# Kernel tuning notes

Measured on AMD Instinct MI355X. Metric: run time of the kernel, lower is better.

The kernel has to match this reference:

```python
import jax, jax.numpy as jnp
import numpy as np

N = 50000
E = 800000
D_IN = 1000
D_H2 = 128  # h_dim * multiple
D_H = 16


def gat_conv(x, src, dst, W, attn_l, attn_r, bias, n):
    """DGL-style GATConv (no dropout, no activation). Returns [n, H, F]."""
    H, F = attn_l.shape
    feat = (x @ W).reshape(n, H, F)                      # [N,H,F]
    el = jnp.sum(feat * attn_l[None], axis=-1)           # [N,H]
    er = jnp.sum(feat * attn_r[None], axis=-1)           # [N,H]
    e = jax.nn.leaky_relu(el[src] + er[dst], 0.2)        # [E,H]
    emax = jax.ops.segment_max(e, dst, num_segments=n)   # [N,H] per-dst softmax max
    ee = jnp.exp(e - emax[dst])                          # [E,H]
    denom = jax.ops.segment_sum(ee, dst, num_segments=n) # [N,H]
    alpha = ee / denom[dst]                              # [E,H]
    msg = feat[src] * alpha[..., None]                   # [E,H,F]
    out = jax.ops.segment_sum(msg, dst, num_segments=n)  # [N,H,F]
    return out + bias.reshape(1, H, F)


def setup_inputs() -> dict:
    key = jax.random.key(0)
    ks = jax.random.split(key, 24)
    rn = lambda k, shp, s=0.05: (jax.random.normal(k, shp, dtype=jnp.float32) * s)
    inp = {
        "x": rn(ks[0], (N, D_IN), 1.0),
        "src": jax.random.randint(ks[1], (E,), 0, N, dtype=jnp.int32),
        "dst": jax.random.randint(ks[2], (E,), 0, N, dtype=jnp.int32),
        "W1": rn(ks[3], (D_IN, D_H2)),
        "al1": rn(ks[4], (1, D_H2)),
        "ar1": rn(ks[5], (1, D_H2)),
        "b1": jnp.zeros((D_H2,), jnp.float32),
        "W2": rn(ks[6], (D_H2, 2 * D_H2)),
        "al2": rn(ks[7], (2, D_H2)),
        "ar2": rn(ks[8], (2, D_H2)),
        "b2": jnp.zeros((2 * D_H2,), jnp.float32),
        "Wm": rn(ks[9], (D_H2, 2 * D_H)),
        "alm": rn(ks[10], (2, D_H)),
        "arm": rn(ks[11], (2, D_H)),
        "bm": jnp.zeros((2 * D_H,), jnp.float32),
        "Wv": rn(ks[12], (D_H2, 2 * D_H)),
        "alv": rn(ks[13], (2, D_H)),
        "arv": rn(ks[14], (2, D_H)),
        "bv": jnp.zeros((2 * D_H,), jnp.float32),
        "eps": rn(ks[15], (N, D_H), 1.0),
    }
    return inp


def reference(x, src, dst, W1, al1, ar1, b1, W2, al2, ar2, b2,
              Wm, alm, arm, bm, Wv, alv, arv, bv, eps):
    n = x.shape[0]
    o = gat_conv(x, src, dst, W1, al1, ar1, b1, n).mean(-2)           # [N,128]
    o = gat_conv(o, src, dst, W2, al2, ar2, b2, n).mean(-2) + o       # residual
    mean = gat_conv(o, src, dst, Wm, alm, arm, bm, n).mean(-2)        # [N,16]
    var = jnp.exp(gat_conv(o, src, dst, Wv, alv, arv, bv, n).mean(-2))
    z = mean + jnp.sqrt(var) * eps                                    # reparameterize
    return z, mean, var
```

## Files before the change

kernel.cpp:

```cpp
#include <hip/hip_runtime.h>
#include <hip/hip_bf16.h>
#include <math.h>

typedef unsigned short u16;
typedef unsigned int u32;
typedef __attribute__((ext_vector_type(8))) __bf16 bf16x8;
typedef __attribute__((ext_vector_type(4))) float f32x4;
typedef __attribute__((ext_vector_type(4))) u32 u32x4;
typedef __attribute__((ext_vector_type(2))) u32 u32x2;

#define NNODES 50000
#define NEDGES 800000

__device__ __forceinline__ float bf2f(u16 u) {
    union { u32 i; float f; } v; v.i = ((u32)u) << 16; return v.f;
}
__device__ __forceinline__ u16 f2bf(float x) {
    union { float f; u32 i; } v; v.f = x;
    u32 r = v.i + 0x7fffu + ((v.i >> 16) & 1u);
    return (u16)(r >> 16);
}
__device__ __forceinline__ float lrelu(float x) { return x >= 0.f ? x : 0.2f * x; }

__global__ __launch_bounds__(256) void k_zero2(int* a, int* b, int count) {
    int i = blockIdx.x * 256 + threadIdx.x;
    if (i < count) { a[i] = 0; b[i] = 0; }
}

__global__ __launch_bounds__(256) void k_count(const int* __restrict__ dst, int* __restrict__ counts, int e) {
    int i = blockIdx.x * 256 + threadIdx.x;
    if (i < e) atomicAdd(&counts[dst[i]], 1);
}

__global__ __launch_bounds__(256) void k_scan1(const int* __restrict__ counts, int* __restrict__ row_ptr,
                                               int* __restrict__ bsums, int n) {
    __shared__ int tmp[256];
    int t = threadIdx.x, i = blockIdx.x * 256 + t;
    int v = (i < n) ? counts[i] : 0;
    tmp[t] = v; __syncthreads();
    for (int off = 1; off < 256; off <<= 1) {
        int x = 0; if (t >= off) x = tmp[t - off];
        __syncthreads(); tmp[t] += x; __syncthreads();
    }
    if (i < n) row_ptr[i] = tmp[t] - v;
    if (t == 255) bsums[blockIdx.x] = tmp[255];
}

__global__ __launch_bounds__(256) void k_scan2(int* bsums, int nb) {
    __shared__ int tmp[256];
    int t = threadIdx.x;
    int v = (t < nb) ? bsums[t] : 0;
    tmp[t] = v; __syncthreads();
    for (int off = 1; off < 256; off <<= 1) {
        int x = 0; if (t >= off) x = tmp[t - off];
        __syncthreads(); tmp[t] += x; __syncthreads();
    }
    if (t < nb) bsums[t] = tmp[t] - v;
}

__global__ __launch_bounds__(256) void k_scan3(int* __restrict__ row_ptr, const int* __restrict__ bsums,
                                               int n, int total) {
    int i = blockIdx.x * 256 + threadIdx.x;
    if (i < n) row_ptr[i] += bsums[blockIdx.x];
    if (i == 0) row_ptr[n] = total;
}

__global__ __launch_bounds__(256) void k_fill(const int* __restrict__ src, const int* __restrict__ dst,
                                              const int* __restrict__ row_ptr, int* __restrict__ cursor,
                                              int* __restrict__ esrc, int e) {
    int i = blockIdx.x * 256 + threadIdx.x;
    if (i < e) {
        int d = dst[i];
        int p = row_ptr[d] + atomicAdd(&cursor[d], 1);
        esrc[p] = src[i];
    }
}

__global__ __launch_bounds__(256) void k_prep(const float* __restrict__ W1, const float* __restrict__ W2,
                                              const float* __restrict__ Wm, const float* __restrict__ Wv,
                                              const float* __restrict__ al2, const float* __restrict__ ar2,
                                              const float* __restrict__ b2,
                                              u16* __restrict__ W1t, u16* __restrict__ Wct,
                                              u16* __restrict__ Bmvt,
                                              float* __restrict__ ul, float* __restrict__ ur,
                                              float* __restrict__ bmean) {
    int b = blockIdx.x, t = threadIdx.x;
    if (b < 500) {
        int i = b * 256 + t;
        int k = i >> 7, n = i & 127;
        W1t[(size_t)n * 1000 + k] = f2bf(W1[i]);
    } else if (b < 628) {
        int i = (b - 500) * 256 + t;
        int f = i >> 8, c = i & 255, h = c >> 7, k = c & 127;
        Wct[i] = f2bf(0.5f * W2[(size_t)k * 256 + h * 128 + f]);
    } else if (b == 628) {
        int h = t >> 7, k = t & 127;
        const float* wrow = W2 + (size_t)k * 256 + h * 128;
        const float* alh = al2 + h * 128;
        const float* arh = ar2 + h * 128;
        float sl = 0.f, sr = 0.f;
        for (int f = 0; f < 128; f += 4) {
            f32x4 w = *(const f32x4*)(wrow + f);
            f32x4 a = *(const f32x4*)(alh + f);
            f32x4 r = *(const f32x4*)(arh + f);
#pragma unroll
            for (int q = 0; q < 4; q++) { sl += w[q] * a[q]; sr += w[q] * r[q]; }
        }
        ul[t] = sl; ur[t] = sr;
        if (t < 128) bmean[t] = 0.5f * (b2[t] + b2[128 + t]);
    } else {
        for (int i = t; i < 64 * 128; i += 256) {
            int c = i >> 7, k = i & 127;
            Bmvt[i] = f2bf(c < 32 ? Wm[(size_t)k * 32 + c] : Wv[(size_t)k * 32 + (c - 32)]);
        }
    }
}

__device__ __forceinline__ void load_af(const float* __restrict__ arow, int k0, int K, bf16x8& a) {
    if (k0 + 8 <= K) {
        f32x4 a0 = *(const f32x4*)(arow + k0);
        f32x4 a1 = *(const f32x4*)(arow + k0 + 4);
#pragma unroll
        for (int j = 0; j < 4; j++) { a[j] = (__bf16)a0[j]; a[4 + j] = (__bf16)a1[j]; }
    } else {
#pragma unroll
        for (int j = 0; j < 8; j++) a[j] = (__bf16)0.f;
    }
}
__device__ __forceinline__ void load_af(const u16* __restrict__ arow, int k0, int K, bf16x8& a) {
    if (k0 + 8 <= K) a = *(const bf16x8*)(arow + k0);
    else {
#pragma unroll
        for (int j = 0; j < 8; j++) a[j] = (__bf16)0.f;
    }
}

template <typename AT, int MODE>
__global__ __launch_bounds__(256) void k_gemm_tiled(const AT* __restrict__ A, const u16* __restrict__ Bt,
                                                    u16* __restrict__ C, int M, int Nn, int K,
                                                    const float* __restrict__ bias,
                                                    const u16* __restrict__ resid,
                                                    const float* __restrict__ al,
                                                    const float* __restrict__ ar,
                                                    float* __restrict__ el, float* __restrict__ er) {
    __shared__ __align__(16) u16 lb[2][128 * 40];
    const int tid = threadIdx.x;
    const int wave = tid >> 6, lane = tid & 63;
    const int m = lane & 15, quad = lane >> 4;
    const int row0 = blockIdx.x * 64 + wave * 16;
    const int col0 = blockIdx.y * 128;

    f32x4 acc[8];
#pragma unroll
    for (int t = 0; t < 8; t++)
#pragma unroll
        for (int r = 0; r < 4; r++) acc[t][r] = 0.f;

    int arr = row0 + m; if (arr > M - 1) arr = M - 1;
    const AT* arow = A + (size_t)arr * K;
    const int scol = tid & 127;
    const int sseg = (tid >> 7) * 16;
    const u16* bcol = Bt + (size_t)(col0 + scol) * K;

    const int nsteps = (K + 31) >> 5;

#pragma unroll
    for (int p = 0; p < 2; ++p) {
        int kl = sseg + p * 8;
        u32x4 v = 0;
        if (kl < K) v = *(const u32x4*)(bcol + kl);
        *(u32x4*)&lb[0][scol * 40 + kl] = v;
    }
    bf16x8 acur, anext;
    load_af(arow, quad * 8, K, acur);
    __syncthreads();

    for (int s = 0; s < nsteps; ++s) {
        const int buf = s & 1;
        if (s + 1 < nsteps) {
            const int k0n = (s + 1) * 32;
            load_af(arow, k0n + quad * 8, K, anext);
#pragma unroll
            for (int p = 0; p < 2; ++p) {
                int kl = sseg + p * 8;
                u32x4 v = 0;
                if (k0n + kl < K) v = *(const u32x4*)(bcol + k0n + kl);
                *(u32x4*)&lb[buf ^ 1][scol * 40 + kl] = v;
            }
        }
#pragma unroll
        for (int t = 0; t < 8; ++t) {
            bf16x8 b = *(const bf16x8*)&lb[buf][(t * 16 + m) * 40 + quad * 8];
            acc[t] = __builtin_amdgcn_mfma_f32_16x16x32_bf16(acur, b, acc[t], 0, 0, 0);
        }
        acur = anext;
        __syncthreads();
    }

#pragma unroll
    for (int r = 0; r < 4; r++) {
        int row = row0 + quad * 4 + r;
        if (MODE == 0) {
            float pe = 0.f, pr = 0.f;
#pragma unroll
            for (int t = 0; t < 8; t++) {
                float a = acc[t][r];
                int c = col0 + t * 16 + m;
                pe += a * al[c]; pr += a * ar[c];
            }
#pragma unroll
            for (int off = 8; off; off >>= 1) { pe += __shfl_xor(pe, off); pr += __shfl_xor(pr, off); }
            if (m == 0 && row < M) { el[row] = pe; er[row] = pr; }
        }
#pragma unroll
        for (int t = 0; t < 8; t++) {
            int col = col0 + t * 16 + m;
            if (row < M) {
                float v = acc[t][r];
                if (MODE == 1) v += bias[col] + bf2f(resid[(size_t)row * Nn + col]);
                C[(size_t)row * Nn + col] = f2bf(v);
            }
        }
    }
}

__global__ __launch_bounds__(64) void k_gemmmv(const u16* __restrict__ A, const u16* __restrict__ Bt,
                                               u16* __restrict__ featmv,
                                               const float* __restrict__ alm, const float* __restrict__ arm,
                                               const float* __restrict__ alv, const float* __restrict__ arv,
                                               float* __restrict__ elm, float* __restrict__ erm,
                                               float* __restrict__ elv, float* __restrict__ erv, int M) {
    int row0 = blockIdx.x * 16;
    int lane = threadIdx.x;
    int m = lane & 15, quad = lane >> 4;
    f32x4 acc[4];
#pragma unroll
    for (int t = 0; t < 4; t++)
#pragma unroll
        for (int r = 0; r < 4; r++) acc[t][r] = 0.f;

    const u16* arow = A + (size_t)(row0 + m) * 128 + quad * 8;
#pragma unroll
    for (int s = 0; s < 4; ++s) {
        bf16x8 a = *(const bf16x8*)(arow + s * 32);
#pragma unroll
        for (int t = 0; t < 4; t++) {
            bf16x8 b = *(const bf16x8*)(Bt + (size_t)(t * 16 + m) * 128 + s * 32 + quad * 8);
            acc[t] = __builtin_amdgcn_mfma_f32_16x16x32_bf16(a, b, acc[t], 0, 0, 0);
        }
    }
#pragma unroll
    for (int r = 0; r < 4; r++) {
        int row = row0 + quad * 4 + r;
#pragma unroll
        for (int t = 0; t < 4; t++) {
            float a = acc[t][r];
            const float* alp = (t < 2) ? alm : alv;
            const float* arp = (t < 2) ? arm : arv;
            float pe = a * alp[(t & 1) * 16 + m];
            float pr = a * arp[(t & 1) * 16 + m];
#pragma unroll
            for (int off = 8; off; off >>= 1) { pe += __shfl_xor(pe, off); pr += __shfl_xor(pr, off); }
            if (m == 0 && row < M) {
                float* elp = (t < 2) ? elm : elv;
                float* erp = (t < 2) ? erm : erv;
                elp[row * 2 + (t & 1)] = pe; erp[row * 2 + (t & 1)] = pr;
            }
            if (row < M) featmv[(size_t)row * 64 + t * 16 + m] = f2bf(a);
        }
    }
}

__global__ __launch_bounds__(256) void k_agg1(const int* __restrict__ row_ptr, const int* __restrict__ esrc,
                                              const u16* __restrict__ feat, const float* __restrict__ el,
                                              const float* __restrict__ er, const float* __restrict__ bias,
                                              const float* __restrict__ ul, const float* __restrict__ ur,
                                              u16* __restrict__ o_bf, float* __restrict__ el2,
                                              float* __restrict__ er2, int n) {
    int wave = threadIdx.x >> 6, lane = threadIdx.x & 63;
    int l = lane & 31;
    int node = blockIdx.x * 8 + wave * 2 + (lane >> 5);
    if (node >= n) node = n - 1;
    int beg = row_ptr[node], deg = row_ptr[node + 1] - beg;
    float erd = er[node];
    int degmax = max(deg, __shfl_xor(deg, 32));
    const int srcb = lane & 32;
    float acc0 = 0.f, acc1 = 0.f, acc2 = 0.f, acc3 = 0.f, den = 0.f;
    for (int off0 = 0; off0 < degmax; off0 += 32) {
        float w = 0.f; int s = 0;
        if (off0 + l < deg) { s = esrc[beg + off0 + l]; w = expf(lrelu(el[s] + erd)); }
        den += w;
        int cnt = min(32, degmax - off0);
        int j = 0;
        for (; j + 4 <= cnt; j += 4) {
            int s0 = __shfl(s, srcb + j),     s1 = __shfl(s, srcb + j + 1);
            int s2 = __shfl(s, srcb + j + 2), s3 = __shfl(s, srcb + j + 3);
            float w0 = __shfl(w, srcb + j),     w1 = __shfl(w, srcb + j + 1);
            float w2 = __shfl(w, srcb + j + 2), w3 = __shfl(w, srcb + j + 3);
            u32x2 p0 = ((const u32x2*)(feat + (size_t)s0 * 128))[l];
            u32x2 p1 = ((const u32x2*)(feat + (size_t)s1 * 128))[l];
            u32x2 p2 = ((const u32x2*)(feat + (size_t)s2 * 128))[l];
            u32x2 p3 = ((const u32x2*)(feat + (size_t)s3 * 128))[l];
            acc0 += w0 * bf2f((u16)(p0.x & 0xffff)) + w1 * bf2f((u16)(p1.x & 0xffff))
                  + w2 * bf2f((u16)(p2.x & 0xffff)) + w3 * bf2f((u16)(p3.x & 0xffff));
            acc1 += w0 * bf2f((u16)(p0.x >> 16)) + w1 * bf2f((u16)(p1.x >> 16))
                  + w2 * bf2f((u16)(p2.x >> 16)) + w3 * bf2f((u16)(p3.x >> 16));
            acc2 += w0 * bf2f((u16)(p0.y & 0xffff)) + w1 * bf2f((u16)(p1.y & 0xffff))
                  + w2 * bf2f((u16)(p2.y & 0xffff)) + w3 * bf2f((u16)(p3.y & 0xffff));
            acc3 += w0 * bf2f((u16)(p0.y >> 16)) + w1 * bf2f((u16)(p1.y >> 16))
                  + w2 * bf2f((u16)(p2.y >> 16)) + w3 * bf2f((u16)(p3.y >> 16));
        }
        for (; j < cnt; ++j) {
            int sj = __shfl(s, srcb + j);
            float wj = __shfl(w, srcb + j);
            u32x2 pv = ((const u32x2*)(feat + (size_t)sj * 128))[l];
            acc0 += wj * bf2f((u16)(pv.x & 0xffff));
            acc1 += wj * bf2f((u16)(pv.x >> 16));
            acc2 += wj * bf2f((u16)(pv.y & 0xffff));
            acc3 += wj * bf2f((u16)(pv.y >> 16));
        }
    }
#pragma unroll
    for (int off = 16; off; off >>= 1) den += __shfl_xor(den, off);
    float inv = (den > 0.f) ? 1.f / den : 0.f;
    const int c0 = 4 * l;
    float o0 = acc0 * inv + bias[c0];
    float o1 = acc1 * inv + bias[c0 + 1];
    float o2 = acc2 * inv + bias[c0 + 2];
    float o3 = acc3 * inv + bias[c0 + 3];
#pragma unroll
    for (int h = 0; h < 2; ++h) {
        const float* ulh = ul + h * 128 + c0;
        const float* urh = ur + h * 128 + c0;
        float pe = o0 * ulh[0] + o1 * ulh[1] + o2 * ulh[2] + o3 * ulh[3];
        float pr = o0 * urh[0] + o1 * urh[1] + o2 * urh[2] + o3 * urh[3];
#pragma unroll
        for (int off = 16; off; off >>= 1) { pe += __shfl_xor(pe, off); pr += __shfl_xor(pr, off); }
        if (l == 0) { el2[node * 2 + h] = pe; er2[node * 2 + h] = pr; }
    }
    u32x2 pv;
    pv.x = (u32)f2bf(o0) | ((u32)f2bf(o1) << 16);
    pv.y = (u32)f2bf(o2) | ((u32)f2bf(o3) << 16);
    ((u32x2*)(o_bf + (size_t)node * 128))[l] = pv;
}

__global__ __launch_bounds__(256) void k_agg2o(const int* __restrict__ row_ptr, const int* __restrict__ esrc,
                                               const u16* __restrict__ o_in, const float* __restrict__ el,
                                               const float* __restrict__ er, u16* __restrict__ agg, int n) {
    int wave = threadIdx.x >> 6, lane = threadIdx.x & 63;
    int l = lane & 31;
    int node = blockIdx.x * 8 + wave * 2 + (lane >> 5);
    if (node >= n) node = n - 1;
    int beg = row_ptr[node], deg = row_ptr[node + 1] - beg;
    float er0 = er[node * 2], er1 = er[node * 2 + 1];
    int degmax = max(deg, __shfl_xor(deg, 32));
    const int srcb = lane & 32;
    float a00 = 0.f, a01 = 0.f, a02 = 0.f, a03 = 0.f;
    float a10 = 0.f, a11 = 0.f, a12 = 0.f, a13 = 0.f;
    float d0 = 0.f, d1 = 0.f;
    for (int off0 = 0; off0 < degmax; off0 += 32) {
        float w0 = 0.f, w1 = 0.f; int s = 0;
        if (off0 + l < deg) {
            s = esrc[beg + off0 + l];
            float2 e2 = *(const float2*)(el + 2 * s);
            w0 = expf(lrelu(e2.x + er0));
            w1 = expf(lrelu(e2.y + er1));
        }
        d0 += w0; d1 += w1;
        int cnt = min(32, degmax - off0);
        int j = 0;
        for (; j + 2 <= cnt; j += 2) {
            int sa = __shfl(s, srcb + j), sb = __shfl(s, srcb + j + 1);
            float w0a = __shfl(w0, srcb + j), w0b = __shfl(w0, srcb + j + 1);
            float w1a = __shfl(w1, srcb + j), w1b = __shfl(w1, srcb + j + 1);
            u32x2 pa = ((const u32x2*)(o_in + (size_t)sa * 128))[l];
            u32x2 pb = ((const u32x2*)(o_in + (size_t)sb * 128))[l];
            float fa0 = bf2f((u16)(pa.x & 0xffff)), fa1 = bf2f((u16)(pa.x >> 16));
            float fa2 = bf2f((u16)(pa.y & 0xffff)), fa3 = bf2f((u16)(pa.y >> 16));
            float fb0 = bf2f((u16)(pb.x & 0xffff)), fb1 = bf2f((u16)(pb.x >> 16));
            float fb2 = bf2f((u16)(pb.y & 0xffff)), fb3 = bf2f((u16)(pb.y >> 16));
            a00 += w0a * fa0 + w0b * fb0;  a01 += w0a * fa1 + w0b * fb1;
            a02 += w0a * fa2 + w0b * fb2;  a03 += w0a * fa3 + w0b * fb3;
            a10 += w1a * fa0 + w1b * fb0;  a11 += w1a * fa1 + w1b * fb1;
            a12 += w1a * fa2 + w1b * fb2;  a13 += w1a * fa3 + w1b * fb3;
        }
        for (; j < cnt; ++j) {
            int sj = __shfl(s, srcb + j);
            float w0j = __shfl(w0, srcb + j), w1j = __shfl(w1, srcb + j);
            u32x2 pv = ((const u32x2*)(o_in + (size_t)sj * 128))[l];
            float f0 = bf2f((u16)(pv.x & 0xffff)), f1 = bf2f((u16)(pv.x >> 16));
            float f2 = bf2f((u16)(pv.y & 0xffff)), f3 = bf2f((u16)(pv.y >> 16));
            a00 += w0j * f0; a01 += w0j * f1; a02 += w0j * f2; a03 += w0j * f3;
            a10 += w1j * f0; a11 += w1j * f1; a12 += w1j * f2; a13 += w1j * f3;
        }
    }
#pragma unroll
    for (int off = 16; off; off >>= 1) { d0 += __shfl_xor(d0, off); d1 += __shfl_xor(d1, off); }
    float i0 = (d0 > 0.f) ? 1.f / d0 : 0.f, i1 = (d1 > 0.f) ? 1.f / d1 : 0.f;
    u32x2 p0, p1;
    p0.x = (u32)f2bf(a00 * i0) | ((u32)f2bf(a01 * i0) << 16);
    p0.y = (u32)f2bf(a02 * i0) | ((u32)f2bf(a03 * i0) << 16);
    p1.x = (u32)f2bf(a10 * i1) | ((u32)f2bf(a11 * i1) << 16);
    p1.y = (u32)f2bf(a12 * i1) | ((u32)f2bf(a13 * i1) << 16);
    u32x2* aw = (u32x2*)(agg + (size_t)node * 256);
    aw[l] = p0;
    aw[32 + l] = p1;
}

__global__ __launch_bounds__(256) void k_aggmv(const int* __restrict__ row_ptr, const int* __restrict__ esrc,
                                               const u16* __restrict__ featmv,
                                               const float* __restrict__ elm, const float* __restrict__ erm,
                                               const float* __restrict__ elv, const float* __restrict__ erv,
                                               const float* __restrict__ bm, const float* __restrict__ bv,
                                               const float* __restrict__ eps, float* __restrict__ out, int n) {
    int wave = threadIdx.x >> 6, lane = threadIdx.x & 63;
    int l = lane & 31;
    int node = blockIdx.x * 8 + wave * 2 + (lane >> 5);
    if (node >= n) node = n - 1;
    int tbl = l >> 4, h = (l >> 3) & 1;
    int beg = row_ptr[node], deg = row_ptr[node + 1] - beg;
    float erm0 = erm[2 * node], erm1 = erm[2 * node + 1];
    float erv0 = erv[2 * node], erv1 = erv[2 * node + 1];
    int degmax = max(deg, __shfl_xor(deg, 32));
    const int srcb = lane & 32;
    float acc0 = 0.f, acc1 = 0.f;
    float dm0 = 0.f, dm1 = 0.f, dv0 = 0.f, dv1 = 0.f;
    for (int off0 = 0; off0 < degmax; off0 += 32) {
        float wm0 = 0.f, wm1 = 0.f, wv0 = 0.f, wv1 = 0.f; int s = 0;
        if (off0 + l < deg) {
            s = esrc[beg + off0 + l];
            float2 em = *(const float2*)(elm + 2 * s);
            float2 ev = *(const float2*)(elv + 2 * s);
            wm0 = expf(lrelu(em.x + erm0));
            wm1 = expf(lrelu(em.y + erm1));
            wv0 = expf(lrelu(ev.x + erv0));
            wv1 = expf(lrelu(ev.y + erv1));
        }
        dm0 += wm0; dm1 += wm1; dv0 += wv0; dv1 += wv1;
        int cnt = min(32, degmax - off0);
        int j = 0;
        for (; j + 2 <= cnt; j += 2) {
            int sa = __shfl(s, srcb + j), sb = __shfl(s, srcb + j + 1);
            float am0 = __shfl(wm0, srcb + j), bm0_ = __shfl(wm0, srcb + j + 1);
            float am1 = __shfl(wm1, srcb + j), bm1_ = __shfl(wm1, srcb + j + 1);
            float av0 = __shfl(wv0, srcb + j), bv0_ = __shfl(wv0, srcb + j + 1);
            float av1 = __shfl(wv1, srcb + j), bv1_ = __shfl(wv1, srcb + j + 1);
            float wa = tbl ? (h ? av1 : av0) : (h ? am1 : am0);
            float wb = tbl ? (h ? bv1_ : bv0_) : (h ? bm1_ : bm0_);
            u32 pa = ((const u32*)(featmv + (size_t)sa * 64))[l];
            u32 pb = ((const u32*)(featmv + (size_t)sb * 64))[l];
            acc0 += wa * bf2f((u16)(pa & 0xffff)) + wb * bf2f((u16)(pb & 0xffff));
            acc1 += wa * bf2f((u16)(pa >> 16)) + wb * bf2f((u16)(pb >> 16));
        }
        for (; j < cnt; ++j) {
            int sj = __shfl(s, srcb + j);
            float b0 = __shfl(wm0, srcb + j);
            float b1 = __shfl(wm1, srcb + j);
            float b2 = __shfl(wv0, srcb + j);
            float b3 = __shfl(wv1, srcb + j);
            float wj = tbl ? (h ? b3 : b2) : (h ? b1 : b0);
            u32 pv = ((const u32*)(featmv + (size_t)sj * 64))[l];
            acc0 += wj * bf2f((u16)(pv & 0xffff));
            acc1 += wj * bf2f((u16)(pv >> 16));
        }
    }
#pragma unroll
    for (int off = 16; off; off >>= 1) {
        dm0 += __shfl_xor(dm0, off); dm1 += __shfl_xor(dm1, off);
        dv0 += __shfl_xor(dv0, off); dv1 += __shfl_xor(dv1, off);
    }
    float den = tbl ? (h ? dv1 : dv0) : (h ? dm1 : dm0);
    float inv = (den > 0.f) ? 1.f / den : 0.f;
    const int fidx0 = (2 * l) & 31;
    float bias0 = tbl ? bv[fidx0] : bm[fidx0];
    float bias1 = tbl ? bv[fidx0 + 1] : bm[fidx0 + 1];
    float outc0 = acc0 * inv + bias0;
    float outc1 = acc1 * inv + bias1;
    float hm0 = 0.5f * (outc0 + __shfl_xor(outc0, 8));
    float hm1 = 0.5f * (outc1 + __shfl_xor(outc1, 8));
    int srcv = srcb + 16 + (l & 7);
    float vp0 = __shfl(hm0, srcv);
    float vp1 = __shfl(hm1, srcv);
    if (l < 8) {
        int f0 = 2 * l;
        float var0 = expf(vp0), var1 = expf(vp1);
        float2 e2 = *(const float2*)(eps + (size_t)node * 16 + f0);
        float z0 = hm0 + sqrtf(var0) * e2.x;
        float z1 = hm1 + sqrtf(var1) * e2.y;
        size_t base = (size_t)node * 16 + f0;
        *(float2*)(out + base) = make_float2(z0, z1);
        *(float2*)(out + (size_t)NNODES * 16 + base) = make_float2(hm0, hm1);
        *(float2*)(out + (size_t)2 * NNODES * 16 + base) = make_float2(var0, var1);
    }
}

extern "C" void kernel_launch(void* const* d_in, const int* in_sizes, int n_in,
                              void* d_out, int out_size, void* d_ws, size_t ws_size,
                              hipStream_t stream) {
    const int N = NNODES, E = NEDGES;
    const float* x   = (const float*)d_in[0];
    const int* src   = (const int*)d_in[1];
    const int* dst   = (const int*)d_in[2];
    const float* W1  = (const float*)d_in[3];
    const float* al1 = (const float*)d_in[4];
    const float* ar1 = (const float*)d_in[5];
    const float* b1  = (const float*)d_in[6];
    const float* W2  = (const float*)d_in[7];
    const float* al2 = (const float*)d_in[8];
    const float* ar2 = (const float*)d_in[9];
    const float* b2  = (const float*)d_in[10];
    const float* Wm  = (const float*)d_in[11];
    const float* alm = (const float*)d_in[12];
    const float* arm = (const float*)d_in[13];
    const float* bm  = (const float*)d_in[14];
    const float* Wv  = (const float*)d_in[15];
    const float* alv = (const float*)d_in[16];
    const float* arv = (const float*)d_in[17];
    const float* bv  = (const float*)d_in[18];
    const float* eps = (const float*)d_in[19];
    float* out = (float*)d_out;

    char* ws = (char*)d_ws;
    size_t off = 0;
    auto take = [&](size_t bytes) { size_t r = off; off += (bytes + 255) & ~(size_t)255; return r; };
    int* counts   = (int*)(ws + take((size_t)N * 4));
    int* cursor   = (int*)(ws + take((size_t)N * 4));
    int* row_ptr  = (int*)(ws + take((size_t)(N + 1) * 4));
    int* bsums    = (int*)(ws + take(256 * 4));
    int* esrc     = (int*)(ws + take((size_t)E * 4));
    u16* W1t      = (u16*)(ws + take((size_t)128 * 1000 * 2));
    u16* Wct      = (u16*)(ws + take((size_t)128 * 256 * 2));
    u16* Bmvt     = (u16*)(ws + take((size_t)64 * 128 * 2));
    float* ul2    = (float*)(ws + take(256 * 4));
    float* ur2    = (float*)(ws + take(256 * 4));
    float* bmean  = (float*)(ws + take(128 * 4));
    float* el1    = (float*)(ws + take((size_t)N * 4));
    float* er1    = (float*)(ws + take((size_t)N * 4));
    float* el2    = (float*)(ws + take((size_t)N * 2 * 4));
    float* er2    = (float*)(ws + take((size_t)N * 2 * 4));
    float* elm    = (float*)(ws + take((size_t)N * 2 * 4));
    float* erm    = (float*)(ws + take((size_t)N * 2 * 4));
    float* elv    = (float*)(ws + take((size_t)N * 2 * 4));
    float* erv    = (float*)(ws + take((size_t)N * 2 * 4));
    u16* o_bf     = (u16*)(ws + take((size_t)N * 128 * 2));
    u16* o2_bf    = (u16*)(ws + take((size_t)N * 128 * 2));
    u16* R        = (u16*)(ws + take((size_t)N * 256 * 2));
    u16* feat1    = R;
    u16* agg      = R;
    u16* featmv   = R;
    (void)ws_size; (void)n_in; (void)in_sizes; (void)out_size;

    const int nb = (N + 255) / 256;
    const int eb = (E + 255) / 256;
    const int wb8 = (N + 7) / 8;
    const int gb = (N + 63) / 64;

    k_prep<<<dim3(630), 256, 0, stream>>>(W1, W2, Wm, Wv, al2, ar2, b2, W1t, Wct, Bmvt, ul2, ur2, bmean);

    k_zero2<<<dim3(nb), 256, 0, stream>>>(counts, cursor, N);
    k_count<<<dim3(eb), 256, 0, stream>>>(dst, counts, E);
    k_scan1<<<dim3(nb), 256, 0, stream>>>(counts, row_ptr, bsums, N);
    k_scan2<<<dim3(1), 256, 0, stream>>>(bsums, nb);
    k_scan3<<<dim3(nb), 256, 0, stream>>>(row_ptr, bsums, N, E);
    k_fill<<<dim3(eb), 256, 0, stream>>>(src, dst, row_ptr, cursor, esrc, E);

    k_gemm_tiled<float, 0><<<dim3(gb, 1), 256, 0, stream>>>(x, W1t, feat1, N, 128, 1000,
                                                            nullptr, nullptr, al1, ar1, el1, er1);
    k_agg1<<<dim3(wb8), 256, 0, stream>>>(row_ptr, esrc, feat1, el1, er1, b1, ul2, ur2,
                                          o_bf, el2, er2, N);

    k_agg2o<<<dim3(wb8), 256, 0, stream>>>(row_ptr, esrc, o_bf, el2, er2, agg, N);
    k_gemm_tiled<u16, 1><<<dim3(gb, 1), 256, 0, stream>>>(agg, Wct, o2_bf, N, 128, 256,
                                                          bmean, o_bf, nullptr, nullptr, nullptr, nullptr);

    k_gemmmv<<<dim3(N / 16), 64, 0, stream>>>(o2_bf, Bmvt, featmv, alm, arm, alv, arv,
                                              elm, erm, elv, erv, N);
    k_aggmv<<<dim3(wb8), 256, 0, stream>>>(row_ptr, esrc, featmv, elm, erm, elv, erv,
                                           bm, bv, eps, out, N);
}
```

Measured before the change: 577.3 us.

## Use direct global-to-LDS loads in GEMM, unroll gather, stage weights in LDS

New measurement: 577.5 us. Within noise of the previous version (+0.0%).

```diff
diff --git a/kernel.cpp b/kernel.cpp
--- a/kernel.cpp
+++ b/kernel.cpp
@@ -21,6 +21,11 @@
     return (u16)(r >> 16);
 }
 __device__ __forceinline__ float lrelu(float x) { return x >= 0.f ? x : 0.2f * x; }
+
+__device__ __forceinline__ void gload_lds16(const u16* g, u16* l) {
+    __builtin_amdgcn_global_load_lds((const __attribute__((address_space(1))) u32*)g,
+                                     (__attribute__((address_space(3))) u32*)l, 16, 0, 0);
+}
 
 __global__ __launch_bounds__(256) void k_zero2(int* a, int* b, int count) {
     int i = blockIdx.x * 256 + threadIdx.x;
@@ -143,7 +148,7 @@
                                                     const float* __restrict__ al,
                                                     const float* __restrict__ ar,
                                                     float* __restrict__ el, float* __restrict__ er) {
-    __shared__ __align__(16) u16 lb[2][128 * 40];
+    __shared__ __align__(16) u16 lb[2][4096];
     const int tid = threadIdx.x;
     const int wave = tid >> 6, lane = tid & 63;
     const int m = lane & 15, quad = lane >> 4;
@@ -158,19 +163,17 @@
 
     int arr = row0 + m; if (arr > M - 1) arr = M - 1;
     const AT* arow = A + (size_t)arr * K;
-    const int scol = tid & 127;
-    const int sseg = (tid >> 7) * 16;
-    const u16* bcol = Bt + (size_t)(col0 + scol) * K;
+    const int colA = (wave & 1) * 64 + lane;
+    const int qb = (wave >> 1) * 2;
+    const u16* bcol = Bt + (size_t)(col0 + colA) * K;
+    u16* lds0 = &lb[0][(qb * 128 + colA) * 8];
+    u16* lds1 = &lb[1][(qb * 128 + colA) * 8];
 
     const int nsteps = (K + 31) >> 5;
 
 #pragma unroll
-    for (int p = 0; p < 2; ++p) {
-        int kl = sseg + p * 8;
-        u32x4 v = 0;
-        if (kl < K) v = *(const u32x4*)(bcol + kl);
-        *(u32x4*)&lb[0][scol * 40 + kl] = v;
-    }
+    for (int p = 0; p < 2; ++p)
+        gload_lds16(bcol + (qb + p) * 8, lds0 + p * 1024);
     bf16x8 acur, anext;
     load_af(arow, quad * 8, K, acur);
     __syncthreads();
@@ -180,17 +183,16 @@
         if (s + 1 < nsteps) {
             const int k0n = (s + 1) * 32;
             load_af(arow, k0n + quad * 8, K, anext);
+            u16* ldsn = buf ? lds0 : lds1;
 #pragma unroll
             for (int p = 0; p < 2; ++p) {
-                int kl = sseg + p * 8;
-                u32x4 v = 0;
-                if (k0n + kl < K) v = *(const u32x4*)(bcol + k0n + kl);
-                *(u32x4*)&lb[buf ^ 1][scol * 40 + kl] = v;
+                int kq = k0n + (qb + p) * 8;
+                if (kq < K) gload_lds16(bcol + kq, ldsn + p * 1024);
             }
         }
 #pragma unroll
         for (int t = 0; t < 8; ++t) {
-            bf16x8 b = *(const bf16x8*)&lb[buf][(t * 16 + m) * 40 + quad * 8];
+            bf16x8 b = *(const bf16x8*)&lb[buf][(quad * 128 + t * 16 + m) * 8];
             acc[t] = __builtin_amdgcn_mfma_f32_16x16x32_bf16(acur, b, acc[t], 0, 0, 0);
         }
         acur = anext;
@@ -369,20 +371,33 @@
         d0 += w0; d1 += w1;
         int cnt = min(32, degmax - off0);
         int j = 0;
-        for (; j + 2 <= cnt; j += 2) {
-            int sa = __shfl(s, srcb + j), sb = __shfl(s, srcb + j + 1);
-            float w0a = __shfl(w0, srcb + j), w0b = __shfl(w0, srcb + j + 1);
-            float w1a = __shfl(w1, srcb + j), w1b = __shfl(w1, srcb + j + 1);
+        for (; j + 4 <= cnt; j += 4) {
+            int sa = __shfl(s, srcb + j),     sb = __shfl(s, srcb + j + 1);
+            int sc = __shfl(s, srcb + j + 2), sd = __shfl(s, srcb + j + 3);
+            float w0a = __shfl(w0, srcb + j),     w0b = __shfl(w0, srcb + j + 1);
+            float w0c = __shfl(w0, srcb + j + 2), w0d = __shfl(w0, srcb + j + 3);
+            float w1a = __shfl(w1, srcb + j),     w1b = __shfl(w1, srcb + j + 1);
+            float w1c = __shfl(w1, srcb + j + 2), w1d = __shfl(w1, srcb + j + 3);
             u32x2 pa = ((const u32x2*)(o_in + (size_t)sa * 128))[l];
             u32x2 pb = ((const u32x2*)(o_in + (size_t)sb * 128))[l];
+            u32x2 pc = ((const u32x2*)(o_in + (size_t)sc * 128))[l];
+            u32x2 pd = ((const u32x2*)(o_in + (size_t)sd * 128))[l];
             float fa0 = bf2f((u16)(pa.x & 0xffff)), fa1 = bf2f((u16)(pa.x >> 16));
             float fa2 = bf2f((u16)(pa.y & 0xffff)), fa3 = bf2f((u16)(pa.y >> 16));
             float fb0 = bf2f((u16)(pb.x & 0xffff)), fb1 = bf2f((u16)(pb.x >> 16));
             float fb2 = bf2f((u16)(pb.y & 0xffff)), fb3 = bf2f((u16)(pb.y >> 16));
-            a00 += w0a * fa0 + w0b * fb0;  a01 += w0a * fa1 + w0b * fb1;
-            a02 += w0a * fa2 + w0b * fb2;  a03 += w0a * fa3 + w0b * fb3;
-            a10 += w1a * fa0 + w1b * fb0;  a11 += w1a * fa1 + w1b * fb1;
-            a12 += w1a * fa2 + w1b * fb2;  a13 += w1a * fa3 + w1b * fb3;
+            float fc0 = bf2f((u16)(pc.x & 0xffff)), fc1 = bf2f((u16)(pc.x >> 16));
+            float fc2 = bf2f((u16)(pc.y & 0xffff)), fc3 = bf2f((u16)(pc.y >> 16));
+            float fd0 = bf2f((u16)(pd.x & 0xffff)), fd1 = bf2f((u16)(pd.x >> 16));
+            float fd2 = bf2f((u16)(pd.y & 0xffff)), fd3 = bf2f((u16)(pd.y >> 16));
+            a00 += w0a * fa0 + w0b * fb0 + w0c * fc0 + w0d * fd0;
+            a01 += w0a * fa1 + w0b * fb1 + w0c * fc1 + w0d * fd1;
+            a02 += w0a * fa2 + w0b * fb2 + w0c * fc2 + w0d * fd2;
+            a03 += w0a * fa3 + w0b * fb3 + w0c * fc3 + w0d * fd3;
+            a10 += w1a * fa0 + w1b * fb0 + w1c * fc0 + w1d * fd0;
+            a11 += w1a * fa1 + w1b * fb1 + w1c * fc1 + w1d * fd1;
+            a12 += w1a * fa2 + w1b * fb2 + w1c * fc2 + w1d * fd2;
+            a13 += w1a * fa3 + w1b * fb3 + w1c * fc3 + w1d * fd3;
         }
         for (; j < cnt; ++j) {
             int sj = __shfl(s, srcb + j);
@@ -413,16 +428,20 @@
                                                const float* __restrict__ elv, const float* __restrict__ erv,
                                                const float* __restrict__ bm, const float* __restrict__ bv,
                                                const float* __restrict__ eps, float* __restrict__ out, int n) {
-    int wave = threadIdx.x >> 6, lane = threadIdx.x & 63;
+    __shared__ float wsm[256 * 4];
+    __shared__ int ssm[256];
+    int tid = threadIdx.x;
+    int wave = tid >> 6, lane = tid & 63;
     int l = lane & 31;
     int node = blockIdx.x * 8 + wave * 2 + (lane >> 5);
     if (node >= n) node = n - 1;
     int tbl = l >> 4, h = (l >> 3) & 1;
+    const int wtype = l >> 3;
     int beg = row_ptr[node], deg = row_ptr[node + 1] - beg;
     float erm0 = erm[2 * node], erm1 = erm[2 * node + 1];
     float erv0 = erv[2 * node], erv1 = erv[2 * node + 1];
     int degmax = max(deg, __shfl_xor(deg, 32));
-    const int srcb = lane & 32;
+    const int bidx = wave * 64 + (lane & 32);
     float acc0 = 0.f, acc1 = 0.f;
     float dm0 = 0.f, dm1 = 0.f, dv0 = 0.f, dv1 = 0.f;
     for (int off0 = 0; off0 < degmax; off0 += 32) {
@@ -437,28 +456,23 @@
             wv1 = expf(lrelu(ev.y + erv1));
         }
         dm0 += wm0; dm1 += wm1; dv0 += wv0; dv1 += wv1;
+        f32x4 wq; wq[0] = wm0; wq[1] = wm1; wq[2] = wv0; wq[3] = wv1;
+        *(f32x4*)&wsm[tid * 4] = wq;
+        ssm[tid] = s;
         int cnt = min(32, degmax - off0);
         int j = 0;
         for (; j + 2 <= cnt; j += 2) {
-            int sa = __shfl(s, srcb + j), sb = __shfl(s, srcb + j + 1);
-            float am0 = __shfl(wm0, srcb + j), bm0_ = __shfl(wm0, srcb + j + 1);
-            float am1 = __shfl(wm1, srcb + j), bm1_ = __shfl(wm1, srcb + j + 1);
-            float av0 = __shfl(wv0, srcb + j), bv0_ = __shfl(wv0, srcb + j + 1);
-            float av1 = __shfl(wv1, srcb + j), bv1_ = __shfl(wv1, srcb + j + 1);
-            float wa = tbl ? (h ? av1 : av0) : (h ? am1 : am0);
-            float wb = tbl ? (h ? bv1_ : bv0_) : (h ? bm1_ : bm0_);
+            int sa = ssm[bidx + j], sb = ssm[bidx + j + 1];
+            float wa = wsm[(bidx + j) * 4 + wtype];
+            float wb = wsm[(bidx + j + 1) * 4 + wtype];
             u32 pa = ((const u32*)(featmv + (size_t)sa * 64))[l];
             u32 pb = ((const u32*)(featmv + (size_t)sb * 64))[l];
             acc0 += wa * bf2f((u16)(pa & 0xffff)) + wb * bf2f((u16)(pb & 0xffff));
             acc1 += wa * bf2f((u16)(pa >> 16)) + wb * bf2f((u16)(pb >> 16));
         }
         for (; j < cnt; ++j) {
-            int sj = __shfl(s, srcb + j);
-            float b0 = __shfl(wm0, srcb + j);
-            float b1 = __shfl(wm1, srcb + j);
-            float b2 = __shfl(wv0, srcb + j);
-            float b3 = __shfl(wv1, srcb + j);
-            float wj = tbl ? (h ? b3 : b2) : (h ? b1 : b0);
+            int sj = ssm[bidx + j];
+            float wj = wsm[(bidx + j) * 4 + wtype];
             u32 pv = ((const u32*)(featmv + (size_t)sj * 64))[l];
             acc0 += wj * bf2f((u16)(pv & 0xffff));
             acc1 += wj * bf2f((u16)(pv >> 16));
@@ -478,7 +492,7 @@
     float outc1 = acc1 * inv + bias1;
     float hm0 = 0.5f * (outc0 + __shfl_xor(outc0, 8));
     float hm1 = 0.5f * (outc1 + __shfl_xor(outc1, 8));
-    int srcv = srcb + 16 + (l & 7);
+    int srcv = (lane & 32) + 16 + (l & 7);
     float vp0 = __shfl(hm0, srcv);
     float vp1 = __shfl(hm1, srcv);
     if (l < 8) {
```
